# Kernel tuning notes

Hardware: AMD Instinct MI355X
Metric: run time of the kernel (lower is better)

Reference implementation:

```python
import jax, jax.numpy as jnp
import numpy as np
from jax import lax

INPUT_SIZE = 64
HIDDEN_SIZE = 4096
OUTPUT_SIZE = 16
SEQ_LEN = 4096
SPECTRAL_RADIUS = 0.95
LEAKY_RATE = 0.9
INPUT_SCALING = 1.0
FEEDBACK_SCALING = 0.1
SPARSITY = 0.1


def setup_inputs() -> dict:
    key = jax.random.key(0)
    ks = jax.random.split(key, 7)
    X = jax.random.normal(ks[0], (SEQ_LEN, INPUT_SIZE), dtype=jnp.float32)
    W_in = jax.random.normal(ks[1], (HIDDEN_SIZE, INPUT_SIZE), dtype=jnp.float32) * INPUT_SCALING
    # sparse reservoir matrix, scaled so spectral radius ~ SPECTRAL_RADIUS
    dense = jax.random.normal(ks[2], (HIDDEN_SIZE, HIDDEN_SIZE), dtype=jnp.float32)
    mask = (jax.random.uniform(ks[3], (HIDDEN_SIZE, HIDDEN_SIZE)) < SPARSITY).astype(jnp.float32)
    # circular-law estimate of spectral radius for sparse gaussian: sqrt(density*N)
    scale = SPECTRAL_RADIUS / np.sqrt(SPARSITY * HIDDEN_SIZE)
    W_res = dense * mask * scale
    b = jax.random.normal(ks[4], (HIDDEN_SIZE,), dtype=jnp.float32)
    W_fb = jax.random.normal(ks[5], (HIDDEN_SIZE, OUTPUT_SIZE), dtype=jnp.float32) * FEEDBACK_SCALING
    W_out = jax.random.normal(ks[6], (OUTPUT_SIZE, HIDDEN_SIZE), dtype=jnp.float32) * 0.01
    return {"X": X, "W_in": W_in, "W_res": W_res, "b": b, "W_fb": W_fb, "W_out": W_out}


def reference(X, W_in, W_res, b, W_fb, W_out):
    """ESN with feedback + leaky integration; Force readout (inference: y = W_out @ s).
    Returns (results [T, O], outputs [T, H]) matching ESNForce.forward."""
    H = W_res.shape[0]
    O = W_out.shape[0]

    def step(carry, x_t):
        s, y = carry  # previous state [H], previous output [O]
        pre = W_in @ x_t + W_res @ s + b + W_fb @ y
        s_new = (1.0 - LEAKY_RATE) * s + LEAKY_RATE * jnp.tanh(pre)
        y_new = W_out @ s_new
        return (s_new, y_new), (y_new, s_new)

    init = (jnp.zeros((H,), dtype=X.dtype), jnp.zeros((O,), dtype=X.dtype))
    _, (results, outputs) = lax.scan(step, init, X)
    return results, outputs
```

## Files before the change

kernel.cpp:

```cpp
#include <hip/hip_runtime.h>
#include <cstdint>

#define NBLK 128
#define BLOCK 1024
#define ROWS 32
#define HDIM 4096
#define IDIM 64
#define ODIM 16
#define TSTEPS 4096
#define PAD 576
#define GMAX 18
#define LEAK 0.9f
#define SU 11
#define SUS 12
#define YU 8

typedef float f32x4 __attribute__((ext_vector_type(4)));

__global__ void init_ws(float* ws) {
    int i = blockIdx.x * blockDim.x + threadIdx.x;
    if (i < (2 * NBLK * SUS + 2 * NBLK * YU) * 4) ws[i] = 0.0f;
}

__global__ __launch_bounds__(BLOCK) void esn_kernel(
    const float* __restrict__ X,
    const float* __restrict__ Win,
    const float* __restrict__ Wres,
    const float* __restrict__ bvec,
    const float* __restrict__ Wfb,
    const float* __restrict__ Wout,
    float* __restrict__ out,
    float* __restrict__ sx,
    float* __restrict__ yx)
{
    __shared__ float          ell_val[ROWS][PAD];
    __shared__ unsigned short ell_idx[ROWS][PAD];
    __shared__ __align__(16) float s_lds[HDIM];
    __shared__ float          win_lds[ROWS][IDIM];
    __shared__ float          wfb_lds[ROWS][ODIM];
    __shared__ __align__(8)  float wout_lds[ROWS][ODIM];
    __shared__ float          b_lds[ROWS];
    __shared__ float          x_lds[IDIM];
    __shared__ float          y_lds[ODIM];
    __shared__ __align__(16) float snew_lds[ROWS];
    __shared__ int            nnz_lds[ROWS];
    __shared__ int            rnds_lds[ROWS];
    __shared__ unsigned short bankCnt[ROWS][32];
    __shared__ unsigned short grpCnt[ROWS][GMAX];

    const int tid   = threadIdx.x;
    const int blk   = blockIdx.x;
    const int rbase = blk * ROWS;

    for (int i = tid; i < ROWS * PAD; i += BLOCK) {
        ell_val[i / PAD][i % PAD] = 0.0f;
        ell_idx[i / PAD][i % PAD] = 0;
    }
    for (int i = tid; i < ROWS * 32; i += BLOCK) bankCnt[i >> 5][i & 31] = 0;
    for (int i = tid; i < ROWS * GMAX; i += BLOCK) grpCnt[i / GMAX][i % GMAX] = 0;

    {
        const int wave = tid >> 6, lane = tid & 63;
        for (int rr = wave * 2; rr < wave * 2 + 2; ++rr) {
            const float* wrow = Wres + (size_t)(rbase + rr) * HDIM;
            int cnt = 0;
            for (int c0 = 0; c0 < HDIM; c0 += 64)
                cnt += __popcll(__ballot(wrow[c0 + lane] != 0.0f));
            if (lane == 0) {
                int nz = cnt < PAD ? cnt : PAD;
                nnz_lds[rr] = nz;
                int gu = (nz + 31) >> 5;
                if (gu < 1) gu = 1;
                if (gu > GMAX) gu = GMAX;
                rnds_lds[rr] = (gu + 1) >> 1;
            }
        }
    }
    __syncthreads();

    {
        const int wave = tid >> 6, lane = tid & 63;
        if (lane == 0 || lane == 32) {
            const int row = wave * 2 + (lane >> 5);
            const int nz  = nnz_lds[row];
            int gu = (nz + 31) >> 5;
            if (gu < 1) gu = 1;
            if (gu > GMAX) gu = GMAX;
            const float* wrow = Wres + (size_t)(rbase + row) * HDIM;
            int placed = 0;
            for (int c = 0; c < HDIM && placed < nz; ++c) {
                const float w = wrow[c];
                if (w != 0.0f) {
                    const int b = c & 31;
                    const int r = bankCnt[row][b];
                    bankCnt[row][b] = (unsigned short)(r + 1);
                    int g = r % gu;
                    int p = grpCnt[row][g];
                    int guard = 0;
                    while (p >= 32 && guard < GMAX) {
                        g = (g + 1 == gu) ? 0 : g + 1;
                        p = grpCnt[row][g];
                        ++guard;
                    }
                    if (p >= 32) break;
                    grpCnt[row][g] = (unsigned short)(p + 1);
                    const int slot = ((g >> 1) << 6) + 2 * p + (g & 1);
                    ell_val[row][slot] = w;
                    ell_idx[row][slot] = (unsigned short)c;
                    ++placed;
                }
            }
        }
    }

    for (int i = tid; i < ROWS * IDIM; i += BLOCK)
        win_lds[i >> 6][i & 63] = Win[(size_t)(rbase + (i >> 6)) * IDIM + (i & 63)];
    for (int i = tid; i < ROWS * ODIM; i += BLOCK)
        wfb_lds[i >> 4][i & 15] = Wfb[(size_t)(rbase + (i >> 4)) * ODIM + (i & 15)];
    for (int i = tid; i < ROWS * ODIM; i += BLOCK)
        wout_lds[i >> 4][i & 15] = Wout[(size_t)(i & 15) * HDIM + rbase + (i >> 4)];
    if (tid < ROWS) b_lds[tid] = bvec[rbase + tid];

    for (int i = tid; i < HDIM; i += BLOCK) s_lds[i] = 0.0f;
    if (tid < ODIM) y_lds[tid] = 0.0f;
    if (tid >= 64 && tid < 128) x_lds[tid - 64] = X[tid - 64];
    __syncthreads();

    float* out_res = out;
    float* out_s   = out + (size_t)TSTEPS * ODIM;

    const int rowB = tid >> 5;
    const int lB   = tid & 31;
    const int RB   = rnds_lds[rowB];

    for (int t = 0; t < TSTEPS; ++t) {
        const unsigned tu = (unsigned)(t + 1);
        const float tagf = __uint_as_float(tu);

        {
            float a0 = 0.0f, a1 = 0.0f;
            for (int k = 0; k < RB; ++k) {
                const int e = (k << 6) + (lB << 1);
                const float2  v  = *(const float2*)&ell_val[rowB][e];
                const ushort2 ix = *(const ushort2*)&ell_idx[rowB][e];
                a0 += v.x * s_lds[ix.x];
                a1 += v.y * s_lds[ix.y];
            }
            float acc = a0 + a1;
            acc += win_lds[rowB][lB] * x_lds[lB] + win_lds[rowB][lB + 32] * x_lds[lB + 32];
            if (lB < ODIM) acc += wfb_lds[rowB][lB] * y_lds[lB];
            acc += __shfl_xor(acc, 16, 32);
            acc += __shfl_xor(acc, 8, 32);
            acc += __shfl_xor(acc, 4, 32);
            acc += __shfl_xor(acc, 2, 32);
            acc += __shfl_xor(acc, 1, 32);
            if (lB == 0) {
                const float pre = acc + b_lds[rowB];
                snew_lds[rowB] = (1.0f - LEAK) * s_lds[rbase + rowB] + LEAK * tanhf(pre);
            }
        }
        __syncthreads();

        const int wv = tid >> 6;
        const int ln = tid & 63;
        if (wv == 0) {
            if (ln >= 16 && ln < 16 + SU) {
                const int j  = ln - 16;
                const int b0 = 3 * j;
                const int b1 = (3 * j + 1 < 32) ? 3 * j + 1 : 31;
                const int b2 = (3 * j + 2 < 32) ? 3 * j + 2 : 31;
                f32x4 v;
                v.x = snew_lds[b0]; v.y = snew_lds[b1]; v.z = snew_lds[b2]; v.w = tagf;
                float* dst = sx + (((size_t)(t & 1) * NBLK + blk) * SUS + j) * 4;
                asm volatile("global_store_dwordx4 %0, %1, off sc0 sc1"
                             :: "v"(dst), "v"(v) : "memory");
            }
            if (ln < YU) {
                float a0 = 0.0f, a1 = 0.0f;
                #pragma unroll
                for (int r = 0; r < ROWS; ++r) {
                    const float2 w = *(const float2*)&wout_lds[r][2 * ln];
                    a0 += w.x * snew_lds[r];
                    a1 += w.y * snew_lds[r];
                }
                f32x4 v; v.x = a0; v.y = a1; v.z = tagf; v.w = 0.0f;
                float* dst = yx + (((size_t)(t & 1) * NBLK + blk) * YU + ln) * 4;
                asm volatile("global_store_dwordx4 %0, %1, off sc0 sc1"
                             :: "v"(dst), "v"(v) : "memory");
            }
            if (ln >= 32 && ln < 40) {
                const int j = ln - 32;
                *(f32x4*)(out_s + (size_t)t * HDIM + rbase + j * 4) =
                    *(const f32x4*)&snew_lds[j * 4];
            }
        } else if (wv == 1) {
            if (t + 1 < TSTEPS) x_lds[ln] = X[(size_t)(t + 1) * IDIM + ln];
            const int u  = ln & 7;
            const int pg = ln >> 3;
            const float* yb = yx + (size_t)(t & 1) * NBLK * YU * 4;
            f32x4 w0,w1,w2,w3,w4,w5,w6,w7,w8,w9,w10,w11,w12,w13,w14,w15;
            for (;;) {
                #define YL(i) asm volatile("global_load_dwordx4 %0, %1, off sc0 sc1" \
                    : "=v"(w##i) : "v"(yb + (((pg << 4) + i) * YU + u) * 4));
                YL(0) YL(1) YL(2) YL(3) YL(4) YL(5) YL(6) YL(7)
                YL(8) YL(9) YL(10) YL(11) YL(12) YL(13) YL(14) YL(15)
                #undef YL
                asm volatile("s_waitcnt vmcnt(0)" ::: "memory");
                __builtin_amdgcn_sched_barrier(0);
                bool ok = __float_as_uint(w0.z) == tu  && __float_as_uint(w1.z) == tu
                       && __float_as_uint(w2.z) == tu  && __float_as_uint(w3.z) == tu
                       && __float_as_uint(w4.z) == tu  && __float_as_uint(w5.z) == tu
                       && __float_as_uint(w6.z) == tu  && __float_as_uint(w7.z) == tu
                       && __float_as_uint(w8.z) == tu  && __float_as_uint(w9.z) == tu
                       && __float_as_uint(w10.z) == tu && __float_as_uint(w11.z) == tu
                       && __float_as_uint(w12.z) == tu && __float_as_uint(w13.z) == tu
                       && __float_as_uint(w14.z) == tu && __float_as_uint(w15.z) == tu;
                if (__all(ok)) break;
            }
            float acc0 = ((w0.x + w1.x) + (w2.x + w3.x)) + ((w4.x + w5.x) + (w6.x + w7.x))
                       + ((w8.x + w9.x) + (w10.x + w11.x)) + ((w12.x + w13.x) + (w14.x + w15.x));
            float acc1 = ((w0.y + w1.y) + (w2.y + w3.y)) + ((w4.y + w5.y) + (w6.y + w7.y))
                       + ((w8.y + w9.y) + (w10.y + w11.y)) + ((w12.y + w13.y) + (w14.y + w15.y));
            acc0 += __shfl_xor(acc0, 8);  acc1 += __shfl_xor(acc1, 8);
            acc0 += __shfl_xor(acc0, 16); acc1 += __shfl_xor(acc1, 16);
            acc0 += __shfl_xor(acc0, 32); acc1 += __shfl_xor(acc1, 32);
            if (ln < 8) {
                if (t + 1 < TSTEPS) { y_lds[2 * u] = acc0; y_lds[2 * u + 1] = acc1; }
                if (blk == 0) {
                    out_res[(size_t)t * ODIM + 2 * u]     = acc0;
                    out_res[(size_t)t * ODIM + 2 * u + 1] = acc1;
                }
            }
        } else {
            if (t + 1 < TSTEPS) {
                const int wi    = wv - 2;
                const int start = (wi < 2) ? wi * 10 : 20 + (wi - 2) * 9;
                const int count = (wi < 2) ? 10 : 9;
                const int U     = count * SU;
                const float* sb = sx + (size_t)(t & 1) * NBLK * SUS * 4;
                const int g0 = ln, g1 = ln + 64;
                const int p0 = g0 / SU, u0 = g0 - p0 * SU;
                const bool h1 = g1 < U;
                const int p1 = g1 / SU, u1 = g1 - p1 * SU;
                const float* a0p = sb + (((start + p0) * SUS) + u0) * 4;
                const float* a1p = sb + (((start + p1) * SUS) + u1) * 4;
                f32x4 v0, v1;
                for (;;) {
                    asm volatile("global_load_dwordx4 %0, %1, off sc0 sc1"
                                 : "=v"(v0) : "v"(a0p));
                    if (h1)
                        asm volatile("global_load_dwordx4 %0, %1, off sc0 sc1"
                                     : "=v"(v1) : "v"(a1p));
                    asm volatile("s_waitcnt vmcnt(0)" ::: "memory");
                    __builtin_amdgcn_sched_barrier(0);
                    bool ok = (__float_as_uint(v0.w) == tu) &&
                              (!h1 || __float_as_uint(v1.w) == tu);
                    if (__all(ok)) break;
                }
                {
                    const int c0 = (start + p0) * 32 + u0 * 3;
                    s_lds[c0] = v0.x; s_lds[c0 + 1] = v0.y;
                    if (u0 != SU - 1) s_lds[c0 + 2] = v0.z;
                }
                if (h1) {
                    const int c1 = (start + p1) * 32 + u1 * 3;
                    s_lds[c1] = v1.x; s_lds[c1 + 1] = v1.y;
                    if (u1 != SU - 1) s_lds[c1 + 2] = v1.z;
                }
            }
        }
        __syncthreads();
    }
}

extern "C" void kernel_launch(void* const* d_in, const int* in_sizes, int n_in,
                              void* d_out, int out_size, void* d_ws, size_t ws_size,
                              hipStream_t stream) {
    (void)in_sizes; (void)n_in; (void)out_size; (void)ws_size;
    const float* X    = (const float*)d_in[0];
    const float* Win  = (const float*)d_in[1];
    const float* Wres = (const float*)d_in[2];
    const float* b    = (const float*)d_in[3];
    const float* Wfb  = (const float*)d_in[4];
    const float* Wout = (const float*)d_in[5];
    float* out = (float*)d_out;
    float* sx  = (float*)d_ws;
    float* yx  = (float*)d_ws + 2 * NBLK * SUS * 4;

    const int words = (2 * NBLK * SUS + 2 * NBLK * YU) * 4;
    init_ws<<<(words + 255) / 256, 256, 0, stream>>>((float*)d_ws);
    esn_kernel<<<NBLK, BLOCK, 0, stream>>>(X, Win, Wres, b, Wfb, Wout, out, sx, yx);
}
```

Measured before the change: 20.09 ms.

## Split reservoir over 256 smaller blocks and publish state per wave via LDS flags

Moves from 128 blocks of 1024 threads to 256 blocks of 512 threads (16 rows each), so each block handles fewer rows per step. Each wave now writes its two new state values and tag straight to global memory, with no block barrier first, and signals wave 0 through workgroup-scope LDS flags. The y-partials are published as one tagged packet per block, and the input X is double-buffered. The intent is a shorter critical path per timestep, paid for by twice as many blocks polling global flags and more cross-block reduction traffic per step.

```diff
diff --git a/kernel.cpp b/kernel.cpp
--- a/kernel.cpp
+++ b/kernel.cpp
@@ -1,9 +1,9 @@
 #include <hip/hip_runtime.h>
 #include <cstdint>
 
-#define NBLK 128
-#define BLOCK 1024
-#define ROWS 32
+#define NBLK 256
+#define BLOCK 512
+#define ROWS 16
 #define HDIM 4096
 #define IDIM 64
 #define ODIM 16
@@ -11,15 +11,14 @@
 #define PAD 576
 #define GMAX 18
 #define LEAK 0.9f
-#define SU 11
-#define SUS 12
-#define YU 8
+#define SUN 8
+#define YUN 8
 
 typedef float f32x4 __attribute__((ext_vector_type(4)));
 
 __global__ void init_ws(float* ws) {
     int i = blockIdx.x * blockDim.x + threadIdx.x;
-    if (i < (2 * NBLK * SUS + 2 * NBLK * YU) * 4) ws[i] = 0.0f;
+    if (i < 2 * NBLK * (SUN + YUN) * 4) ws[i] = 0.0f;
 }
 
 __global__ __launch_bounds__(BLOCK) void esn_kernel(
@@ -38,11 +37,13 @@
     __shared__ __align__(16) float s_lds[HDIM];
     __shared__ float          win_lds[ROWS][IDIM];
     __shared__ float          wfb_lds[ROWS][ODIM];
-    __shared__ __align__(8)  float wout_lds[ROWS][ODIM];
+    __shared__ float          wout_lds[ROWS][ODIM];
     __shared__ float          b_lds[ROWS];
-    __shared__ float          x_lds[IDIM];
-    __shared__ float          y_lds[ODIM];
-    __shared__ __align__(16) float snew_lds[ROWS];
+    __shared__ float          x_lds[2][IDIM];
+    __shared__ __align__(16) float y_lds[ODIM];
+    __shared__ float          snew_lds[ROWS];
+    __shared__ __align__(16) float ytmp[ODIM];
+    __shared__ unsigned       snflag[8];
     __shared__ int            nnz_lds[ROWS];
     __shared__ int            rnds_lds[ROWS];
     __shared__ unsigned short bankCnt[ROWS][32];
@@ -123,7 +124,8 @@
 
     for (int i = tid; i < HDIM; i += BLOCK) s_lds[i] = 0.0f;
     if (tid < ODIM) y_lds[tid] = 0.0f;
-    if (tid >= 64 && tid < 128) x_lds[tid - 64] = X[tid - 64];
+    if (tid < IDIM) x_lds[0][tid] = X[tid];
+    if (tid < 8) snflag[tid] = 0u;
     __syncthreads();
 
     float* out_res = out;
@@ -131,6 +133,8 @@
 
     const int rowB = tid >> 5;
     const int lB   = tid & 31;
+    const int wv   = tid >> 6;
+    const int ln   = tid & 63;
     const int RB   = rnds_lds[rowB];
 
     for (int t = 0; t < TSTEPS; ++t) {
@@ -138,6 +142,7 @@
         const float tagf = __uint_as_float(tu);
 
         {
+            const float* xb = x_lds[t & 1];
             float a0 = 0.0f, a1 = 0.0f;
             for (int k = 0; k < RB; ++k) {
                 const int e = (k << 6) + (lB << 1);
@@ -147,126 +152,138 @@
                 a1 += v.y * s_lds[ix.y];
             }
             float acc = a0 + a1;
-            acc += win_lds[rowB][lB] * x_lds[lB] + win_lds[rowB][lB + 32] * x_lds[lB + 32];
+            acc += win_lds[rowB][lB] * xb[lB] + win_lds[rowB][lB + 32] * xb[lB + 32];
             if (lB < ODIM) acc += wfb_lds[rowB][lB] * y_lds[lB];
             acc += __shfl_xor(acc, 16, 32);
             acc += __shfl_xor(acc, 8, 32);
             acc += __shfl_xor(acc, 4, 32);
             acc += __shfl_xor(acc, 2, 32);
             acc += __shfl_xor(acc, 1, 32);
+            float sn = 0.0f;
             if (lB == 0) {
                 const float pre = acc + b_lds[rowB];
-                snew_lds[rowB] = (1.0f - LEAK) * s_lds[rbase + rowB] + LEAK * tanhf(pre);
-            }
-        }
-        __syncthreads();
-
-        const int wv = tid >> 6;
-        const int ln = tid & 63;
-        if (wv == 0) {
-            if (ln >= 16 && ln < 16 + SU) {
-                const int j  = ln - 16;
-                const int b0 = 3 * j;
-                const int b1 = (3 * j + 1 < 32) ? 3 * j + 1 : 31;
-                const int b2 = (3 * j + 2 < 32) ? 3 * j + 2 : 31;
-                f32x4 v;
-                v.x = snew_lds[b0]; v.y = snew_lds[b1]; v.z = snew_lds[b2]; v.w = tagf;
-                float* dst = sx + (((size_t)(t & 1) * NBLK + blk) * SUS + j) * 4;
+                sn = (1.0f - LEAK) * s_lds[rbase + rowB] + LEAK * tanhf(pre);
+                snew_lds[rowB] = sn;
+            }
+            const float sn1 = __shfl(sn, 32);
+            if (ln == 0) {
+                f32x4 v; v.x = sn; v.y = sn1; v.z = tagf; v.w = 0.0f;
+                float* dst = sx + (((size_t)(t & 1) * NBLK + blk) * SUN + wv) * 4;
                 asm volatile("global_store_dwordx4 %0, %1, off sc0 sc1"
                              :: "v"(dst), "v"(v) : "memory");
-            }
-            if (ln < YU) {
-                float a0 = 0.0f, a1 = 0.0f;
+                float2 o2; o2.x = sn; o2.y = sn1;
+                *(float2*)(out_s + (size_t)t * HDIM + rbase + 2 * wv) = o2;
+                __hip_atomic_store(&snflag[wv], tu, __ATOMIC_RELEASE,
+                                   __HIP_MEMORY_SCOPE_WORKGROUP);
+            }
+        }
+
+        if (wv == 0) {
+            for (;;) {
+                unsigned f = (ln < 8)
+                    ? __hip_atomic_load(&snflag[ln], __ATOMIC_ACQUIRE, __HIP_MEMORY_SCOPE_WORKGROUP)
+                    : tu;
+                if (__all(f >= tu)) break;
+            }
+            if (ln < ODIM) {
+                float yo = 0.0f;
                 #pragma unroll
-                for (int r = 0; r < ROWS; ++r) {
-                    const float2 w = *(const float2*)&wout_lds[r][2 * ln];
-                    a0 += w.x * snew_lds[r];
-                    a1 += w.y * snew_lds[r];
-                }
-                f32x4 v; v.x = a0; v.y = a1; v.z = tagf; v.w = 0.0f;
-                float* dst = yx + (((size_t)(t & 1) * NBLK + blk) * YU + ln) * 4;
+                for (int r = 0; r < ROWS; ++r) yo += wout_lds[r][ln] * snew_lds[r];
+                ytmp[ln] = yo;
+            }
+            asm volatile("s_waitcnt lgkmcnt(0)" ::: "memory");
+            __builtin_amdgcn_sched_barrier(0);
+            float* ybw = yx + ((size_t)(t & 1) * NBLK + blk) * YUN * 4;
+            if (ln < 4) {
+                f32x4 dd = *(const f32x4*)&ytmp[ln * 4];
                 asm volatile("global_store_dwordx4 %0, %1, off sc0 sc1"
-                             :: "v"(dst), "v"(v) : "memory");
-            }
-            if (ln >= 32 && ln < 40) {
-                const int j = ln - 32;
-                *(f32x4*)(out_s + (size_t)t * HDIM + rbase + j * 4) =
-                    *(const f32x4*)&snew_lds[j * 4];
+                             :: "v"(ybw + ln * 4), "v"(dd) : "memory");
+            }
+            asm volatile("s_waitcnt vmcnt(0)" ::: "memory");
+            if (ln == 0) {
+                f32x4 tgv; tgv.x = tagf; tgv.y = tagf; tgv.z = tagf; tgv.w = tagf;
+                asm volatile("global_store_dwordx4 %0, %1, off sc0 sc1"
+                             :: "v"(ybw + 16), "v"(tgv) : "memory");
             }
         } else if (wv == 1) {
-            if (t + 1 < TSTEPS) x_lds[ln] = X[(size_t)(t + 1) * IDIM + ln];
-            const int u  = ln & 7;
-            const int pg = ln >> 3;
-            const float* yb = yx + (size_t)(t & 1) * NBLK * YU * 4;
-            f32x4 w0,w1,w2,w3,w4,w5,w6,w7,w8,w9,w10,w11,w12,w13,w14,w15;
+            if (t + 1 < TSTEPS) x_lds[(t + 1) & 1][ln] = X[(size_t)(t + 1) * IDIM + ln];
+            const float* yb = yx + (size_t)(t & 1) * NBLK * YUN * 4;
+            const int p0 = ln, p1 = ln + 64, p2 = ln + 128, p3 = ln + 192;
+            f32x4 tg0, tg1, tg2, tg3;
             for (;;) {
-                #define YL(i) asm volatile("global_load_dwordx4 %0, %1, off sc0 sc1" \
-                    : "=v"(w##i) : "v"(yb + (((pg << 4) + i) * YU + u) * 4));
-                YL(0) YL(1) YL(2) YL(3) YL(4) YL(5) YL(6) YL(7)
-                YL(8) YL(9) YL(10) YL(11) YL(12) YL(13) YL(14) YL(15)
-                #undef YL
+                asm volatile("global_load_dwordx4 %0, %1, off sc0 sc1" : "=v"(tg0) : "v"(yb + (p0 * YUN + 4) * 4));
+                asm volatile("global_load_dwordx4 %0, %1, off sc0 sc1" : "=v"(tg1) : "v"(yb + (p1 * YUN + 4) * 4));
+                asm volatile("global_load_dwordx4 %0, %1, off sc0 sc1" : "=v"(tg2) : "v"(yb + (p2 * YUN + 4) * 4));
+                asm volatile("global_load_dwordx4 %0, %1, off sc0 sc1" : "=v"(tg3) : "v"(yb + (p3 * YUN + 4) * 4));
                 asm volatile("s_waitcnt vmcnt(0)" ::: "memory");
                 __builtin_amdgcn_sched_barrier(0);
-                bool ok = __float_as_uint(w0.z) == tu  && __float_as_uint(w1.z) == tu
-                       && __float_as_uint(w2.z) == tu  && __float_as_uint(w3.z) == tu
-                       && __float_as_uint(w4.z) == tu  && __float_as_uint(w5.z) == tu
-                       && __float_as_uint(w6.z) == tu  && __float_as_uint(w7.z) == tu
-                       && __float_as_uint(w8.z) == tu  && __float_as_uint(w9.z) == tu
-                       && __float_as_uint(w10.z) == tu && __float_as_uint(w11.z) == tu
-                       && __float_as_uint(w12.z) == tu && __float_as_uint(w13.z) == tu
-                       && __float_as_uint(w14.z) == tu && __float_as_uint(w15.z) == tu;
+                bool ok = __float_as_uint(tg0.x) == tu && __float_as_uint(tg1.x) == tu
+                       && __float_as_uint(tg2.x) == tu && __float_as_uint(tg3.x) == tu;
                 if (__all(ok)) break;
             }
-            float acc0 = ((w0.x + w1.x) + (w2.x + w3.x)) + ((w4.x + w5.x) + (w6.x + w7.x))
-                       + ((w8.x + w9.x) + (w10.x + w11.x)) + ((w12.x + w13.x) + (w14.x + w15.x));
-            float acc1 = ((w0.y + w1.y) + (w2.y + w3.y)) + ((w4.y + w5.y) + (w6.y + w7.y))
-                       + ((w8.y + w9.y) + (w10.y + w11.y)) + ((w12.y + w13.y) + (w14.y + w15.y));
-            acc0 += __shfl_xor(acc0, 8);  acc1 += __shfl_xor(acc1, 8);
-            acc0 += __shfl_xor(acc0, 16); acc1 += __shfl_xor(acc1, 16);
-            acc0 += __shfl_xor(acc0, 32); acc1 += __shfl_xor(acc1, 32);
-            if (ln < 8) {
-                if (t + 1 < TSTEPS) { y_lds[2 * u] = acc0; y_lds[2 * u + 1] = acc1; }
+            f32x4 d00,d01,d02,d03,d10,d11,d12,d13,d20,d21,d22,d23,d30,d31,d32,d33;
+            #define LDY(r, p, j) asm volatile("global_load_dwordx4 %0, %1, off sc0 sc1" \
+                : "=v"(r) : "v"(yb + ((p) * YUN + (j)) * 4))
+            LDY(d00,p0,0); LDY(d01,p0,1); LDY(d02,p0,2); LDY(d03,p0,3);
+            LDY(d10,p1,0); LDY(d11,p1,1); LDY(d12,p1,2); LDY(d13,p1,3);
+            LDY(d20,p2,0); LDY(d21,p2,1); LDY(d22,p2,2); LDY(d23,p2,3);
+            LDY(d30,p3,0); LDY(d31,p3,1); LDY(d32,p3,2); LDY(d33,p3,3);
+            #undef LDY
+            asm volatile("s_waitcnt vmcnt(0)" ::: "memory");
+            __builtin_amdgcn_sched_barrier(0);
+            f32x4 a0 = (d00 + d10) + (d20 + d30);
+            f32x4 a1 = (d01 + d11) + (d21 + d31);
+            f32x4 a2 = (d02 + d12) + (d22 + d32);
+            f32x4 a3 = (d03 + d13) + (d23 + d33);
+            #pragma unroll
+            for (int m = 1; m < 64; m <<= 1) {
+                #pragma unroll
+                for (int c = 0; c < 4; ++c) {
+                    a0[c] += __shfl_xor(a0[c], m);
+                    a1[c] += __shfl_xor(a1[c], m);
+                    a2[c] += __shfl_xor(a2[c], m);
+                    a3[c] += __shfl_xor(a3[c], m);
+                }
+            }
+            if (ln == 0) {
+                if (t + 1 < TSTEPS) {
+                    *(f32x4*)&y_lds[0]  = a0; *(f32x4*)&y_lds[4]  = a1;
+                    *(f32x4*)&y_lds[8]  = a2; *(f32x4*)&y_lds[12] = a3;
+                }
                 if (blk == 0) {
-                    out_res[(size_t)t * ODIM + 2 * u]     = acc0;
-                    out_res[(size_t)t * ODIM + 2 * u + 1] = acc1;
+                    f32x4* orp = (f32x4*)(out_res + (size_t)t * ODIM);
+                    orp[0] = a0; orp[1] = a1; orp[2] = a2; orp[3] = a3;
                 }
             }
         } else {
             if (t + 1 < TSTEPS) {
-                const int wi    = wv - 2;
-                const int start = (wi < 2) ? wi * 10 : 20 + (wi - 2) * 9;
-                const int count = (wi < 2) ? 10 : 9;
-                const int U     = count * SU;
-                const float* sb = sx + (size_t)(t & 1) * NBLK * SUS * 4;
-                const int g0 = ln, g1 = ln + 64;
-                const int p0 = g0 / SU, u0 = g0 - p0 * SU;
-                const bool h1 = g1 < U;
-                const int p1 = g1 / SU, u1 = g1 - p1 * SU;
-                const float* a0p = sb + (((start + p0) * SUS) + u0) * 4;
-                const float* a1p = sb + (((start + p1) * SUS) + u1) * 4;
-                f32x4 v0, v1;
+                const float* sb = sx + (size_t)(t & 1) * NBLK * SUN * 4;
+                const int cl = (wv - 2) * 64 + ln;
+                const bool h5 = cl < 128;
+                f32x4 v0, v1, v2, v3, v4, v5;
                 for (;;) {
-                    asm volatile("global_load_dwordx4 %0, %1, off sc0 sc1"
-                                 : "=v"(v0) : "v"(a0p));
-                    if (h1)
-                        asm volatile("global_load_dwordx4 %0, %1, off sc0 sc1"
-                                     : "=v"(v1) : "v"(a1p));
+                    asm volatile("global_load_dwordx4 %0, %1, off sc0 sc1" : "=v"(v0) : "v"(sb + (size_t)cl * 4));
+                    asm volatile("global_load_dwordx4 %0, %1, off sc0 sc1" : "=v"(v1) : "v"(sb + (size_t)(cl +  384) * 4));
+                    asm volatile("global_load_dwordx4 %0, %1, off sc0 sc1" : "=v"(v2) : "v"(sb + (size_t)(cl +  768) * 4));
+                    asm volatile("global_load_dwordx4 %0, %1, off sc0 sc1" : "=v"(v3) : "v"(sb + (size_t)(cl + 1152) * 4));
+                    asm volatile("global_load_dwordx4 %0, %1, off sc0 sc1" : "=v"(v4) : "v"(sb + (size_t)(cl + 1536) * 4));
+                    if (h5)
+                        asm volatile("global_load_dwordx4 %0, %1, off sc0 sc1" : "=v"(v5) : "v"(sb + (size_t)(cl + 1920) * 4));
                     asm volatile("s_waitcnt vmcnt(0)" ::: "memory");
                     __builtin_amdgcn_sched_barrier(0);
-                    bool ok = (__float_as_uint(v0.w) == tu) &&
-                              (!h1 || __float_as_uint(v1.w) == tu);
+                    bool ok = __float_as_uint(v0.z) == tu && __float_as_uint(v1.z) == tu
+                           && __float_as_uint(v2.z) == tu && __float_as_uint(v3.z) == tu
+                           && __float_as_uint(v4.z) == tu
+                           && (!h5 || __float_as_uint(v5.z) == tu);
                     if (__all(ok)) break;
                 }
-                {
-                    const int c0 = (start + p0) * 32 + u0 * 3;
-                    s_lds[c0] = v0.x; s_lds[c0 + 1] = v0.y;
-                    if (u0 != SU - 1) s_lds[c0 + 2] = v0.z;
-                }
-                if (h1) {
-                    const int c1 = (start + p1) * 32 + u1 * 3;
-                    s_lds[c1] = v1.x; s_lds[c1 + 1] = v1.y;
-                    if (u1 != SU - 1) s_lds[c1 + 2] = v1.z;
-                }
+                #define SCAT(v, U) { const int p_ = (U) >> 3, u_ = (U) & 7;          \
+                    float2 s2_; s2_.x = (v).x; s2_.y = (v).y;                         \
+                    *(float2*)&s_lds[p_ * ROWS + 2 * u_] = s2_; }
+                SCAT(v0, cl); SCAT(v1, cl + 384); SCAT(v2, cl + 768);
+                SCAT(v3, cl + 1152); SCAT(v4, cl + 1536);
+                if (h5) SCAT(v5, cl + 1920);
+                #undef SCAT
             }
         }
         __syncthreads();
@@ -285,9 +302,9 @@
     const float* Wout = (const float*)d_in[5];
     float* out = (float*)d_out;
     float* sx  = (float*)d_ws;
-    float* yx  = (float*)d_ws + 2 * NBLK * SUS * 4;
-
-    const int words = (2 * NBLK * SUS + 2 * NBLK * YU) * 4;
+    float* yx  = (float*)d_ws + 2 * NBLK * SUN * 4;
+
+    const int words = 2 * NBLK * (SUN + YUN) * 4;
     init_ws<<<(words + 255) / 256, 256, 0, stream>>>((float*)d_ws);
     esn_kernel<<<NBLK, BLOCK, 0, stream>>>(X, Win, Wres, b, Wfb, Wout, out, sx, yx);
 }
```

New measurement: 36.83 ms. 1.83x slower.

## Double-buffer state in LDS and replace mid-step barrier with per-row flags

Applied to the files above, without the earlier changes.

Double-buffers the shared state, input and feedback arrays by step parity, so writers of next-step data cannot race readers of the current step. The first __syncthreads in each step is replaced by per-row workgroup-scope release flags that wave 0 spin-waits on. Other waves can then move straight to polling remote blocks' data without waiting for every row to finish. This removes one block-wide barrier per step but adds LDS atomic spinning and doubles the state buffer's LDS footprint.

```diff
diff --git a/kernel.cpp b/kernel.cpp
--- a/kernel.cpp
+++ b/kernel.cpp
@@ -35,22 +35,27 @@
 {
     __shared__ float          ell_val[ROWS][PAD];
     __shared__ unsigned short ell_idx[ROWS][PAD];
-    __shared__ __align__(16) float s_lds[HDIM];
+    __shared__ __align__(16) float s_lds[2][HDIM];
     __shared__ float          win_lds[ROWS][IDIM];
     __shared__ float          wfb_lds[ROWS][ODIM];
     __shared__ __align__(8)  float wout_lds[ROWS][ODIM];
     __shared__ float          b_lds[ROWS];
-    __shared__ float          x_lds[IDIM];
-    __shared__ float          y_lds[ODIM];
+    __shared__ float          x_lds[2][IDIM];
+    __shared__ float          y_lds[2][ODIM];
     __shared__ __align__(16) float snew_lds[ROWS];
+    __shared__ unsigned       snflag[ROWS];
     __shared__ int            nnz_lds[ROWS];
     __shared__ int            rnds_lds[ROWS];
-    __shared__ unsigned short bankCnt[ROWS][32];
-    __shared__ unsigned short grpCnt[ROWS][GMAX];
+    __shared__ unsigned char  bankCnt[ROWS][32];
+    __shared__ unsigned char  grpCnt[ROWS][GMAX];
 
     const int tid   = threadIdx.x;
     const int blk   = blockIdx.x;
     const int rbase = blk * ROWS;
+    const int rowB  = tid >> 5;
+    const int lB    = tid & 31;
+    const int wv    = tid >> 6;
+    const int ln    = tid & 63;
 
     for (int i = tid; i < ROWS * PAD; i += BLOCK) {
         ell_val[i / PAD][i % PAD] = 0.0f;
@@ -58,15 +63,15 @@
     }
     for (int i = tid; i < ROWS * 32; i += BLOCK) bankCnt[i >> 5][i & 31] = 0;
     for (int i = tid; i < ROWS * GMAX; i += BLOCK) grpCnt[i / GMAX][i % GMAX] = 0;
+    if (tid < ROWS) snflag[tid] = 0u;
 
     {
-        const int wave = tid >> 6, lane = tid & 63;
-        for (int rr = wave * 2; rr < wave * 2 + 2; ++rr) {
+        for (int rr = wv * 2; rr < wv * 2 + 2; ++rr) {
             const float* wrow = Wres + (size_t)(rbase + rr) * HDIM;
             int cnt = 0;
             for (int c0 = 0; c0 < HDIM; c0 += 64)
-                cnt += __popcll(__ballot(wrow[c0 + lane] != 0.0f));
-            if (lane == 0) {
+                cnt += __popcll(__ballot(wrow[c0 + ln] != 0.0f));
+            if (ln == 0) {
                 int nz = cnt < PAD ? cnt : PAD;
                 nnz_lds[rr] = nz;
                 int gu = (nz + 31) >> 5;
@@ -79,9 +84,8 @@
     __syncthreads();
 
     {
-        const int wave = tid >> 6, lane = tid & 63;
-        if (lane == 0 || lane == 32) {
-            const int row = wave * 2 + (lane >> 5);
+        if (ln == 0 || ln == 32) {
+            const int row = wv * 2 + (ln >> 5);
             const int nz  = nnz_lds[row];
             int gu = (nz + 31) >> 5;
             if (gu < 1) gu = 1;
@@ -93,7 +97,7 @@
                 if (w != 0.0f) {
                     const int b = c & 31;
                     const int r = bankCnt[row][b];
-                    bankCnt[row][b] = (unsigned short)(r + 1);
+                    bankCnt[row][b] = (unsigned char)(r + 1);
                     int g = r % gu;
                     int p = grpCnt[row][g];
                     int guard = 0;
@@ -103,7 +107,7 @@
                         ++guard;
                     }
                     if (p >= 32) break;
-                    grpCnt[row][g] = (unsigned short)(p + 1);
+                    grpCnt[row][g] = (unsigned char)(p + 1);
                     const int slot = ((g >> 1) << 6) + 2 * p + (g & 1);
                     ell_val[row][slot] = w;
                     ell_idx[row][slot] = (unsigned short)c;
@@ -121,34 +125,34 @@
         wout_lds[i >> 4][i & 15] = Wout[(size_t)(i & 15) * HDIM + rbase + (i >> 4)];
     if (tid < ROWS) b_lds[tid] = bvec[rbase + tid];
 
-    for (int i = tid; i < HDIM; i += BLOCK) s_lds[i] = 0.0f;
-    if (tid < ODIM) y_lds[tid] = 0.0f;
-    if (tid >= 64 && tid < 128) x_lds[tid - 64] = X[tid - 64];
+    for (int i = tid; i < HDIM; i += BLOCK) s_lds[0][i] = 0.0f;
+    if (tid < ODIM) y_lds[0][tid] = 0.0f;
+    if (tid >= 64 && tid < 128) x_lds[0][tid - 64] = X[tid - 64];
     __syncthreads();
 
     float* out_res = out;
     float* out_s   = out + (size_t)TSTEPS * ODIM;
-
-    const int rowB = tid >> 5;
-    const int lB   = tid & 31;
-    const int RB   = rnds_lds[rowB];
+    const int RB = rnds_lds[rowB];
 
     for (int t = 0; t < TSTEPS; ++t) {
         const unsigned tu = (unsigned)(t + 1);
         const float tagf = __uint_as_float(tu);
+        const int cur = t & 1, nxt = cur ^ 1;
 
         {
+            const float* sc = s_lds[cur];
             float a0 = 0.0f, a1 = 0.0f;
             for (int k = 0; k < RB; ++k) {
                 const int e = (k << 6) + (lB << 1);
                 const float2  v  = *(const float2*)&ell_val[rowB][e];
                 const ushort2 ix = *(const ushort2*)&ell_idx[rowB][e];
-                a0 += v.x * s_lds[ix.x];
-                a1 += v.y * s_lds[ix.y];
+                a0 += v.x * sc[ix.x];
+                a1 += v.y * sc[ix.y];
             }
             float acc = a0 + a1;
-            acc += win_lds[rowB][lB] * x_lds[lB] + win_lds[rowB][lB + 32] * x_lds[lB + 32];
-            if (lB < ODIM) acc += wfb_lds[rowB][lB] * y_lds[lB];
+            acc += win_lds[rowB][lB] * x_lds[cur][lB]
+                 + win_lds[rowB][lB + 32] * x_lds[cur][lB + 32];
+            if (lB < ODIM) acc += wfb_lds[rowB][lB] * y_lds[cur][lB];
             acc += __shfl_xor(acc, 16, 32);
             acc += __shfl_xor(acc, 8, 32);
             acc += __shfl_xor(acc, 4, 32);
@@ -156,14 +160,19 @@
             acc += __shfl_xor(acc, 1, 32);
             if (lB == 0) {
                 const float pre = acc + b_lds[rowB];
-                snew_lds[rowB] = (1.0f - LEAK) * s_lds[rbase + rowB] + LEAK * tanhf(pre);
+                snew_lds[rowB] = (1.0f - LEAK) * sc[rbase + rowB] + LEAK * tanhf(pre);
+                __hip_atomic_store(&snflag[rowB], tu, __ATOMIC_RELEASE,
+                                   __HIP_MEMORY_SCOPE_WORKGROUP);
             }
         }
-        __syncthreads();
-
-        const int wv = tid >> 6;
-        const int ln = tid & 63;
+
         if (wv == 0) {
+            for (;;) {
+                unsigned f = (ln < ROWS)
+                    ? __hip_atomic_load(&snflag[ln], __ATOMIC_ACQUIRE, __HIP_MEMORY_SCOPE_WORKGROUP)
+                    : tu;
+                if (__all(f >= tu)) break;
+            }
             if (ln >= 16 && ln < 16 + SU) {
                 const int j  = ln - 16;
                 const int b0 = 3 * j;
@@ -171,7 +180,7 @@
                 const int b2 = (3 * j + 2 < 32) ? 3 * j + 2 : 31;
                 f32x4 v;
                 v.x = snew_lds[b0]; v.y = snew_lds[b1]; v.z = snew_lds[b2]; v.w = tagf;
-                float* dst = sx + (((size_t)(t & 1) * NBLK + blk) * SUS + j) * 4;
+                float* dst = sx + (((size_t)cur * NBLK + blk) * SUS + j) * 4;
                 asm volatile("global_store_dwordx4 %0, %1, off sc0 sc1"
                              :: "v"(dst), "v"(v) : "memory");
             }
@@ -184,7 +193,7 @@
                     a1 += w.y * snew_lds[r];
                 }
                 f32x4 v; v.x = a0; v.y = a1; v.z = tagf; v.w = 0.0f;
-                float* dst = yx + (((size_t)(t & 1) * NBLK + blk) * YU + ln) * 4;
+                float* dst = yx + (((size_t)cur * NBLK + blk) * YU + ln) * 4;
                 asm volatile("global_store_dwordx4 %0, %1, off sc0 sc1"
                              :: "v"(dst), "v"(v) : "memory");
             }
@@ -194,10 +203,10 @@
                     *(const f32x4*)&snew_lds[j * 4];
             }
         } else if (wv == 1) {
-            if (t + 1 < TSTEPS) x_lds[ln] = X[(size_t)(t + 1) * IDIM + ln];
+            if (t + 1 < TSTEPS) x_lds[nxt][ln] = X[(size_t)(t + 1) * IDIM + ln];
             const int u  = ln & 7;
             const int pg = ln >> 3;
-            const float* yb = yx + (size_t)(t & 1) * NBLK * YU * 4;
+            const float* yb = yx + (size_t)cur * NBLK * YU * 4;
             f32x4 w0,w1,w2,w3,w4,w5,w6,w7,w8,w9,w10,w11,w12,w13,w14,w15;
             for (;;) {
                 #define YL(i) asm volatile("global_load_dwordx4 %0, %1, off sc0 sc1" \
@@ -225,7 +234,7 @@
             acc0 += __shfl_xor(acc0, 16); acc1 += __shfl_xor(acc1, 16);
             acc0 += __shfl_xor(acc0, 32); acc1 += __shfl_xor(acc1, 32);
             if (ln < 8) {
-                if (t + 1 < TSTEPS) { y_lds[2 * u] = acc0; y_lds[2 * u + 1] = acc1; }
+                if (t + 1 < TSTEPS) { y_lds[nxt][2 * u] = acc0; y_lds[nxt][2 * u + 1] = acc1; }
                 if (blk == 0) {
                     out_res[(size_t)t * ODIM + 2 * u]     = acc0;
                     out_res[(size_t)t * ODIM + 2 * u + 1] = acc1;
@@ -237,7 +246,7 @@
                 const int start = (wi < 2) ? wi * 10 : 20 + (wi - 2) * 9;
                 const int count = (wi < 2) ? 10 : 9;
                 const int U     = count * SU;
-                const float* sb = sx + (size_t)(t & 1) * NBLK * SUS * 4;
+                const float* sb = sx + (size_t)cur * NBLK * SUS * 4;
                 const int g0 = ln, g1 = ln + 64;
                 const int p0 = g0 / SU, u0 = g0 - p0 * SU;
                 const bool h1 = g1 < U;
@@ -257,15 +266,16 @@
                               (!h1 || __float_as_uint(v1.w) == tu);
                     if (__all(ok)) break;
                 }
+                float* sd = s_lds[nxt];
                 {
                     const int c0 = (start + p0) * 32 + u0 * 3;
-                    s_lds[c0] = v0.x; s_lds[c0 + 1] = v0.y;
-                    if (u0 != SU - 1) s_lds[c0 + 2] = v0.z;
+                    sd[c0] = v0.x; sd[c0 + 1] = v0.y;
+                    if (u0 != SU - 1) sd[c0 + 2] = v0.z;
                 }
                 if (h1) {
                     const int c1 = (start + p1) * 32 + u1 * 3;
-                    s_lds[c1] = v1.x; s_lds[c1 + 1] = v1.y;
-                    if (u1 != SU - 1) s_lds[c1 + 2] = v1.z;
+                    sd[c1] = v1.x; sd[c1 + 1] = v1.y;
+                    if (u1 != SU - 1) sd[c1 + 2] = v1.z;
                 }
             }
         }
```

After: 21.43 ms. 1.07x slower.
